# Kernel tuning notes

Measured on AMD Instinct MI355X. Metric: run time of the kernel, lower is better.

The kernel has to match this reference:

```python
import jax, jax.numpy as jnp
import numpy as np

B, N, C, H = 2, 2048, 1024, 16
D = C // H          # head_dim = 64
HALF = D // 2       # 32 complex pairs per head


def setup_inputs() -> dict:
    key = jax.random.key(0)
    k1, k2, k3, k4 = jax.random.split(key, 4)
    x = jax.random.normal(k1, (B, N, C), dtype=jnp.float32)
    # 0.02 init scale keeps softmax logits in a sane range
    qkv_w = jax.random.normal(k2, (3 * C, C), dtype=jnp.float32) * 0.02
    proj_w = jax.random.normal(k3, (C, C), dtype=jnp.float32) * 0.02
    proj_b = jax.random.normal(k4, (C,), dtype=jnp.float32) * 0.02
    # standard RoPE frequencies: theta = 10000^{-2i/D}
    inv_freq = 1.0 / (10000.0 ** (jnp.arange(0, D, 2, dtype=jnp.float32) / D))
    angles = jnp.arange(N, dtype=jnp.float32)[:, None] * inv_freq[None, :]  # [N, HALF]
    return {
        "x": x, "qkv_w": qkv_w, "proj_w": proj_w, "proj_b": proj_b,
        "freqs_cos": jnp.cos(angles), "freqs_sin": jnp.sin(angles),
    }


def _rope(t, cos, sin):
    # t: [B, N, H, D]; cos/sin: [N, HALF] -> broadcast as [1, N, 1, HALF]
    tr = t.reshape(B, N, H, HALF, 2)
    t_re, t_im = tr[..., 0], tr[..., 1]
    c = cos[None, :, None, :]
    s = sin[None, :, None, :]
    o_re = t_re * c - t_im * s
    o_im = t_re * s + t_im * c
    return jnp.stack([o_re, o_im], axis=-1).reshape(B, N, H, D)


def reference(x, qkv_w, proj_w, proj_b, freqs_cos, freqs_sin):
    scale = D ** -0.5
    qkv = x @ qkv_w.T                              # [B, N, 3C] (no bias: qkv_bias=False)
    qkv = qkv.reshape(B, N, 3, H, D)
    q, k, v = qkv[:, :, 0], qkv[:, :, 1], qkv[:, :, 2]  # [B, N, H, D]
    q = _rope(q, freqs_cos, freqs_sin)
    k = _rope(k, freqs_cos, freqs_sin)
    scores = jnp.einsum("bqhd,bkhd->bhqk", q, k) * scale
    attn = jax.nn.softmax(scores, axis=-1)         # dropout p=0.0 -> identity
    out = jnp.einsum("bhqk,bkhd->bqhd", attn, v).reshape(B, N, C)
    return out @ proj_w.T + proj_b
```

## Files before the change

### kernel.cpp

```cpp
#include <hip/hip_runtime.h>
#include <hip/hip_bf16.h>

#define B_ 2
#define N_ 2048
#define C_ 1024
#define H_ 16
#define D_ 64
#define HALF_ 32

typedef __attribute__((ext_vector_type(8))) __bf16 bf16x8;
typedef __attribute__((ext_vector_type(8))) unsigned short u16x8;
typedef __attribute__((ext_vector_type(4))) float f32x4;
typedef __attribute__((ext_vector_type(16))) float f32x16;

__device__ __forceinline__ unsigned short f2bf(float f) {
  union { float f; unsigned u; } v; v.f = f;
  unsigned r = v.u + 0x7FFFu + ((v.u >> 16) & 1u);
  return (unsigned short)(r >> 16);
}

__device__ __forceinline__ unsigned cvt_pk_bf16(float lo, float hi) {
  unsigned r;
  asm("v_cvt_pk_bf16_f32 %0, %1, %2" : "=v"(r) : "v"(lo), "v"(hi));
  return r;
}

__device__ __forceinline__ void gload_lds16(const void* g, void* l) {
  __builtin_amdgcn_global_load_lds(
      (const __attribute__((address_space(1))) void*)g,
      (__attribute__((address_space(3))) void*)l, 16, 0, 0);
}

__global__ __launch_bounds__(256) void cast_f32_bf16(const float* __restrict__ in,
                                                     unsigned short* __restrict__ out,
                                                     int n4) {
  int i = blockIdx.x * 256 + threadIdx.x;
  if (i >= n4) return;
  float4 v = reinterpret_cast<const float4*>(in)[i];
  ushort4 o;
  o.x = f2bf(v.x); o.y = f2bf(v.y); o.z = f2bf(v.z); o.w = f2bf(v.w);
  reinterpret_cast<ushort4*>(out)[i] = o;
}

template <int EPI>
__global__ __launch_bounds__(256) void gemm_bt(
    const unsigned short* __restrict__ A, const unsigned short* __restrict__ Bw,
    int M, int Nn, int K,
    float* __restrict__ Cout, const float* __restrict__ bias,
    unsigned short* __restrict__ qo, unsigned short* __restrict__ ko,
    unsigned short* __restrict__ vto,
    const float* __restrict__ cosT, const float* __restrict__ sinT) {
  __shared__ __align__(16) unsigned short As[128][64];
  __shared__ __align__(16) unsigned short Bs[128][64];
  const int tid = threadIdx.x;
  const int lane = tid & 63;
  const int wid = tid >> 6;
  const int wm = wid >> 1, wn = wid & 1;
  const int l15 = lane & 15;
  const int g = lane >> 4;
  const int m0 = blockIdx.x * 128;
  const int n0 = blockIdx.y * 128;

  const int srow = wid * 8 + (lane >> 3);
  const int scol = (lane & 7) * 8;

  f32x4 acc[4][4] = {};

  const int nK = K >> 6;
  for (int kt = 0; kt < nK; ++kt) {
    __syncthreads();
#pragma unroll
    for (int j = 0; j < 4; ++j) {
      gload_lds16(&A[(size_t)(m0 + j * 32 + srow) * K + kt * 64 + scol],
                  &As[j * 32 + wid * 8][0]);
      gload_lds16(&Bw[(size_t)(n0 + j * 32 + srow) * K + kt * 64 + scol],
                  &Bs[j * 32 + wid * 8][0]);
    }
    __syncthreads();
#pragma unroll
    for (int kk = 0; kk < 2; ++kk) {
      bf16x8 af[4], bfv[4];
#pragma unroll
      for (int m = 0; m < 4; ++m)
        af[m] = *reinterpret_cast<const bf16x8*>(&As[wm * 64 + m * 16 + l15][kk * 32 + g * 8]);
#pragma unroll
      for (int n = 0; n < 4; ++n)
        bfv[n] = *reinterpret_cast<const bf16x8*>(&Bs[wn * 64 + n * 16 + l15][kk * 32 + g * 8]);
#pragma unroll
      for (int m = 0; m < 4; ++m)
#pragma unroll
        for (int n = 0; n < 4; ++n)
          acc[m][n] = __builtin_amdgcn_mfma_f32_16x16x32_bf16(af[m], bfv[n], acc[m][n], 0, 0, 0);
    }
  }

  if constexpr (EPI == 0) {
#pragma unroll
    for (int n = 0; n < 4; ++n) {
      int col = n0 + wn * 64 + n * 16 + l15;
      float bv = bias[col];
#pragma unroll
      for (int m = 0; m < 4; ++m) {
        int rbase = m0 + wm * 64 + m * 16 + g * 4;
#pragma unroll
        for (int r = 0; r < 4; ++r)
          Cout[(size_t)(rbase + r) * Nn + col] = acc[m][n][r] + bv;
      }
    }
  } else {
    const int which = n0 >> 10;
    if (which == 2) {
#pragma unroll
      for (int m = 0; m < 4; ++m)
#pragma unroll
        for (int n = 0; n < 4; ++n) {
          int col = n0 + wn * 64 + n * 16 + l15;
          int hc = col & 1023;
          int hh = hc >> 6, d = hc & 63;
          int row0 = m0 + wm * 64 + m * 16 + g * 4;
          int seq0 = row0 & (N_ - 1), bb = row0 >> 11;
          ushort4 pk;
          pk.x = f2bf(acc[m][n][0]); pk.y = f2bf(acc[m][n][1]);
          pk.z = f2bf(acc[m][n][2]); pk.w = f2bf(acc[m][n][3]);
          *reinterpret_cast<ushort4*>(
              &vto[(((size_t)bb * H_ + hh) * D_ + d) * N_ + seq0]) = pk;
        }
    } else {
      unsigned short* dst = (which == 0) ? qo : ko;
      const float qscale = (which == 0) ? 0.125f * 1.44269504f : 1.0f;
#pragma unroll
      for (int m = 0; m < 4; ++m)
#pragma unroll
        for (int n = 0; n < 4; ++n)
#pragma unroll
          for (int r = 0; r < 4; ++r) {
            int col = n0 + wn * 64 + n * 16 + l15;
            int row = m0 + wm * 64 + m * 16 + g * 4 + r;
            float val = acc[m][n][r];
            float partner = __shfl_xor(val, 1);
            int hc = col & 1023;
            int hh = hc >> 6, d = hc & 63;
            int seq = row & (N_ - 1), bb = row >> 11;
            float cs = cosT[seq * HALF_ + (d >> 1)];
            float sn = sinT[seq * HALF_ + (d >> 1)];
            float res = (d & 1) ? (partner * sn + val * cs) : (val * cs - partner * sn);
            res *= qscale;
            dst[(((size_t)bb * H_ + hh) * N_ + seq) * D_ + d] = f2bf(res);
          }
    }
  }
}

__global__ __launch_bounds__(512) void attn_kernel(
    const unsigned short* __restrict__ q,
    const unsigned short* __restrict__ k,
    const unsigned short* __restrict__ vt,
    unsigned short* __restrict__ o) {
  __shared__ __align__(16) unsigned short Kl[2][64][64];
  __shared__ __align__(16) unsigned short Vl[2][64][64];

  const int tid = threadIdx.x;
  const int lane = tid & 63;
  const int w = tid >> 6;
  const int l31 = lane & 31;
  const int hi = lane >> 5;

  const int bid = blockIdx.x;
  const int nat = (bid & 7) * 32 + (bid >> 3);
  const int qt = nat & 7;
  const int bh = nat >> 3;
  const int b = bh >> 4, h = bh & 15;

  const size_t hk = (size_t)bh * N_ * D_;
  const size_t hv = (size_t)bh * D_ * N_;
  const int qrow = qt * 256 + w * 32 + l31;

  bf16x8 qf[4];
#pragma unroll
  for (int kt = 0; kt < 4; ++kt)
    qf[kt] = *reinterpret_cast<const bf16x8*>(
        &q[hk + (size_t)qrow * D_ + kt * 16 + hi * 8]);

  const int prow = tid >> 3;
  const int pchk = tid & 7;
  const int r7 = prow & 7;
  const int swz = (pchk ^ r7) * 8;
  const int vchunk0 = (pchk >> 1) * 2;
  const int vhalf = (pchk & 1) * 4;
  const int vpos0 = ((vchunk0 ^ r7) << 3) + vhalf;
  const int vpos1 = (((vchunk0 + 1) ^ r7) << 3) + vhalf;

  u16x8 kr, vr;
  auto issue = [&](int t) {
    kr = *reinterpret_cast<const u16x8*>(&k[hk + (size_t)(t * 64 + prow) * D_ + pchk * 8]);
    vr = *reinterpret_cast<const u16x8*>(&vt[hv + (size_t)prow * N_ + t * 64 + pchk * 8]);
  };
  auto commit = [&](int buf) {
    *reinterpret_cast<u16x8*>(&Kl[buf][prow][swz]) = kr;
    union { u16x8 v; ushort4 h[2]; } uv;
    uv.v = vr;
    *reinterpret_cast<ushort4*>(&Vl[buf][prow][vpos0]) = uv.h[0];
    *reinterpret_cast<ushort4*>(&Vl[buf][prow][vpos1]) = uv.h[1];
  };

  issue(0);
  commit(0);
  __syncthreads();

  f32x16 accO[2] = {};
  float mrun = -1e30f, lrun = 0.f;
  const int b7 = l31 & 7;

  const int NT = N_ / 64;
  for (int t = 0; t < NT; ++t) {
    const int cur = t & 1;
    if (t + 1 < NT) issue(t + 1);

    f32x16 s[2] = {};
    __builtin_amdgcn_s_setprio(1);
#pragma unroll
    for (int kb = 0; kb < 2; ++kb)
#pragma unroll
      for (int kt = 0; kt < 4; ++kt) {
        bf16x8 kf = *reinterpret_cast<const bf16x8*>(
            &Kl[cur][kb * 32 + l31][(((kt * 2 + hi) ^ b7)) * 8]);
        s[kb] = __builtin_amdgcn_mfma_f32_32x32x16_bf16(kf, qf[kt], s[kb], 0, 0, 0);
      }
    __builtin_amdgcn_s_setprio(0);

    float mloc[16];
#pragma unroll
    for (int i = 0; i < 16; ++i) mloc[i] = fmaxf(s[0][i], s[1][i]);
#pragma unroll
    for (int st = 8; st > 0; st >>= 1)
#pragma unroll
      for (int i = 0; i < 8; ++i)
        if (i < st) mloc[i] = fmaxf(mloc[i], mloc[i + st]);
    float mx;
    {
      unsigned ua = __float_as_uint(mloc[0]), ub = ua;
      auto r = __builtin_amdgcn_permlane32_swap(ua, ub, false, false);
      mx = fmaxf(__uint_as_float(r[0]), __uint_as_float(r[1]));
    }

    float mnew = fmaxf(mrun, mx);
    if (!__all(mx - mrun <= 8.0f)) {
      float fac = __builtin_exp2f(mrun - mnew);
      lrun *= fac;
#pragma unroll
      for (int db = 0; db < 2; ++db)
#pragma unroll
        for (int i = 0; i < 16; ++i) accO[db][i] *= fac;
      mrun = mnew;
    }

#pragma unroll
    for (int kb = 0; kb < 2; ++kb)
#pragma unroll
      for (int i = 0; i < 16; ++i) s[kb][i] = __builtin_exp2f(s[kb][i] - mrun);

    float sloc[16];
#pragma unroll
    for (int i = 0; i < 16; ++i) sloc[i] = s[0][i] + s[1][i];
#pragma unroll
    for (int st = 8; st > 0; st >>= 1)
#pragma unroll
      for (int i = 0; i < 8; ++i)
        if (i < st) sloc[i] += sloc[i + st];
    {
      unsigned ua = __float_as_uint(sloc[0]), ub = ua;
      auto r = __builtin_amdgcn_permlane32_swap(ua, ub, false, false);
      lrun += __uint_as_float(r[0]) + __uint_as_float(r[1]);
    }

    bf16x8 PA[4];
#pragma unroll
    for (int kvc = 0; kvc < 4; ++kvc) {
      const int kb = kvc >> 1, base = (kvc & 1) * 8;
      union { unsigned u[4]; bf16x8 v; } pa;
#pragma unroll
      for (int wd = 0; wd < 4; ++wd)
        pa.u[wd] = cvt_pk_bf16(s[kb][base + 2 * wd], s[kb][base + 2 * wd + 1]);
      PA[kvc] = pa.v;
    }

    __builtin_amdgcn_s_setprio(1);
#pragma unroll
    for (int db = 0; db < 2; ++db)
#pragma unroll
      for (int kvc = 0; kvc < 4; ++kvc) {
        bf16x8 vf = *reinterpret_cast<const bf16x8*>(
            &Vl[cur][db * 32 + l31][(((kvc * 2 + hi) ^ b7)) * 8]);
        accO[db] = __builtin_amdgcn_mfma_f32_32x32x16_bf16(vf, PA[kvc], accO[db], 0, 0, 0);
      }
    __builtin_amdgcn_s_setprio(0);

    if (t + 1 < NT) commit(cur ^ 1);
    __syncthreads();
  }

  float rl = 1.0f / lrun;
  const size_t obase = ((size_t)b * N_ + qrow) * C_ + h * 64;
#pragma unroll
  for (int db = 0; db < 2; ++db)
#pragma unroll
    for (int rg = 0; rg < 4; ++rg) {
      ushort4 pk;
      pk.x = f2bf(accO[db][rg * 4 + 0] * rl);
      pk.y = f2bf(accO[db][rg * 4 + 1] * rl);
      pk.z = f2bf(accO[db][rg * 4 + 2] * rl);
      pk.w = f2bf(accO[db][rg * 4 + 3] * rl);
      *reinterpret_cast<ushort4*>(&o[obase + db * 32 + rg * 8 + hi * 4]) = pk;
    }
}

extern "C" void kernel_launch(void* const* d_in, const int* in_sizes, int n_in,
                              void* d_out, int out_size, void* d_ws, size_t ws_size,
                              hipStream_t stream) {
  const float* x      = (const float*)d_in[0];
  const float* qkv_w  = (const float*)d_in[1];
  const float* proj_w = (const float*)d_in[2];
  const float* proj_b = (const float*)d_in[3];
  const float* cosT   = (const float*)d_in[4];
  const float* sinT   = (const float*)d_in[5];
  float* out = (float*)d_out;

  unsigned short* xb     = (unsigned short*)d_ws;
  unsigned short* wqkvb  = xb + (size_t)4096 * 1024;
  unsigned short* wprojb = wqkvb + (size_t)3072 * 1024;
  unsigned short* qb     = wprojb + (size_t)1024 * 1024;
  unsigned short* kb     = qb + (size_t)32 * 2048 * 64;
  unsigned short* vtb    = kb + (size_t)32 * 2048 * 64;
  unsigned short* ab     = vtb + (size_t)32 * 2048 * 64;

  cast_f32_bf16<<<4096, 256, 0, stream>>>(x, xb, 4096 * 1024 / 4);
  cast_f32_bf16<<<3072, 256, 0, stream>>>(qkv_w, wqkvb, 3072 * 1024 / 4);
  cast_f32_bf16<<<1024, 256, 0, stream>>>(proj_w, wprojb, 1024 * 1024 / 4);

  dim3 g1(4096 / 128, 3072 / 128);
  gemm_bt<1><<<g1, 256, 0, stream>>>(xb, wqkvb, 4096, 3072, 1024,
                                     nullptr, nullptr, qb, kb, vtb, cosT, sinT);

  attn_kernel<<<256, 512, 0, stream>>>(qb, kb, vtb, ab);

  dim3 g3(4096 / 128, 1024 / 128);
  gemm_bt<0><<<g3, 256, 0, stream>>>(ab, wprojb, 4096, 1024, 1024,
                                     out, proj_b, nullptr, nullptr, nullptr,
                                     nullptr, nullptr);
}
```

Before: 152.5 us.

## Stage K/V tiles via direct global-to-LDS loads and halve attention block size

Replaces the register-staged K/V prefetch (global load into registers, then LDS store after compute) with direct global-to-LDS 16-byte loads issued into the alternate buffer. V transpose output is written with a permuted sequence order so the V tile matches the swizzled LDS layout without per-lane repacking. The attention kernel now uses 256-thread blocks covering 128 query rows, with 512 blocks instead of 256. This should cut VGPR pressure and LDS-store instructions and improve occupancy and load balance. In exchange each K/V tile is loaded twice as often overall.

```diff
diff --git a/kernel.cpp b/kernel.cpp
--- a/kernel.cpp
+++ b/kernel.cpp
@@ -119,11 +119,12 @@
           int hh = hc >> 6, d = hc & 63;
           int row0 = m0 + wm * 64 + m * 16 + g * 4;
           int seq0 = row0 & (N_ - 1), bb = row0 >> 11;
+          int seqP = (seq0 & ~12) | ((seq0 & 4) << 1) | ((seq0 & 8) >> 1);
           ushort4 pk;
           pk.x = f2bf(acc[m][n][0]); pk.y = f2bf(acc[m][n][1]);
           pk.z = f2bf(acc[m][n][2]); pk.w = f2bf(acc[m][n][3]);
           *reinterpret_cast<ushort4*>(
-              &vto[(((size_t)bb * H_ + hh) * D_ + d) * N_ + seq0]) = pk;
+              &vto[(((size_t)bb * H_ + hh) * D_ + d) * N_ + seqP]) = pk;
         }
     } else {
       unsigned short* dst = (which == 0) ? qo : ko;
@@ -151,7 +152,7 @@
   }
 }
 
-__global__ __launch_bounds__(512) void attn_kernel(
+__global__ __launch_bounds__(256) void attn_kernel(
     const unsigned short* __restrict__ q,
     const unsigned short* __restrict__ k,
     const unsigned short* __restrict__ vt,
@@ -166,14 +167,14 @@
   const int hi = lane >> 5;
 
   const int bid = blockIdx.x;
-  const int nat = (bid & 7) * 32 + (bid >> 3);
-  const int qt = nat & 7;
-  const int bh = nat >> 3;
+  const int nat = (bid & 7) * 64 + (bid >> 3);
+  const int qt = nat & 15;
+  const int bh = nat >> 4;
   const int b = bh >> 4, h = bh & 15;
 
   const size_t hk = (size_t)bh * N_ * D_;
   const size_t hv = (size_t)bh * D_ * N_;
-  const int qrow = qt * 256 + w * 32 + l31;
+  const int qrow = qt * 128 + w * 32 + l31;
 
   bf16x8 qf[4];
 #pragma unroll
@@ -181,30 +182,21 @@
     qf[kt] = *reinterpret_cast<const bf16x8*>(
         &q[hk + (size_t)qrow * D_ + kt * 16 + hi * 8]);
 
-  const int prow = tid >> 3;
-  const int pchk = tid & 7;
-  const int r7 = prow & 7;
-  const int swz = (pchk ^ r7) * 8;
-  const int vchunk0 = (pchk >> 1) * 2;
-  const int vhalf = (pchk & 1) * 4;
-  const int vpos0 = ((vchunk0 ^ r7) << 3) + vhalf;
-  const int vpos1 = (((vchunk0 + 1) ^ r7) << 3) + vhalf;
-
-  u16x8 kr, vr;
-  auto issue = [&](int t) {
-    kr = *reinterpret_cast<const u16x8*>(&k[hk + (size_t)(t * 64 + prow) * D_ + pchk * 8]);
-    vr = *reinterpret_cast<const u16x8*>(&vt[hv + (size_t)prow * N_ + t * 64 + pchk * 8]);
+  const int lrow = lane >> 3;
+  const int lchk = lane & 7;
+  const int sc = (lchk ^ lrow) * 8;
+  auto stage = [&](int t, int buf) {
+#pragma unroll
+    for (int gi = 0; gi < 2; ++gi) {
+      const int row = w * 16 + gi * 8 + lrow;
+      gload_lds16(&k[hk + (size_t)(t * 64 + row) * D_ + sc],
+                  &Kl[buf][w * 16 + gi * 8][0]);
+      gload_lds16(&vt[hv + (size_t)row * N_ + t * 64 + sc],
+                  &Vl[buf][w * 16 + gi * 8][0]);
+    }
   };
-  auto commit = [&](int buf) {
-    *reinterpret_cast<u16x8*>(&Kl[buf][prow][swz]) = kr;
-    union { u16x8 v; ushort4 h[2]; } uv;
-    uv.v = vr;
-    *reinterpret_cast<ushort4*>(&Vl[buf][prow][vpos0]) = uv.h[0];
-    *reinterpret_cast<ushort4*>(&Vl[buf][prow][vpos1]) = uv.h[1];
-  };
-
-  issue(0);
-  commit(0);
+
+  stage(0, 0);
   __syncthreads();
 
   f32x16 accO[2] = {};
@@ -214,7 +206,7 @@
   const int NT = N_ / 64;
   for (int t = 0; t < NT; ++t) {
     const int cur = t & 1;
-    if (t + 1 < NT) issue(t + 1);
+    if (t + 1 < NT) stage(t + 1, cur ^ 1);
 
     f32x16 s[2] = {};
     __builtin_amdgcn_s_setprio(1);
@@ -295,7 +287,6 @@
       }
     __builtin_amdgcn_s_setprio(0);
 
-    if (t + 1 < NT) commit(cur ^ 1);
     __syncthreads();
   }
 
@@ -341,7 +332,7 @@
   gemm_bt<1><<<g1, 256, 0, stream>>>(xb, wqkvb, 4096, 3072, 1024,
                                      nullptr, nullptr, qb, kb, vtb, cosT, sinT);
 
-  attn_kernel<<<256, 512, 0, stream>>>(qb, kb, vtb, ab);
+  attn_kernel<<<512, 256, 0, stream>>>(qb, kb, vtb, ab);
 
   dim3 g3(4096 / 128, 1024 / 128);
   gemm_bt<0><<<g3, 256, 0, stream>>>(ab, wprojb, 4096, 1024, 1024,
```

Result: slower. 165.4 us (+8.5%).
